# Kernel tuning notes

Hardware: AMD Instinct MI355X
Metric: run time of the kernel (lower is better)

The kernel has to match this reference:

```python
import jax, jax.numpy as jnp
import numpy as np

B, S, HID = 2, 2048, 768
H, D = 12, 64  # heads_num, per_head_size


def setup_inputs() -> dict:
    key0 = jax.random.key(0)
    ks = jax.random.split(key0, 12)
    inp = {
        "key": jax.random.normal(ks[0], (B, S, HID), jnp.float32),
        "value": jax.random.normal(ks[1], (B, S, HID), jnp.float32),
        "query": jax.random.normal(ks[2], (B, S, HID), jnp.float32),
        "mask": jnp.zeros((B, 1, S, S), jnp.float32),  # additive mask
        "position_bias": jax.random.normal(ks[3], (1, H, S, S), jnp.float32),
        "prev_attn": jax.random.normal(ks[4], (B, H, S, S), jnp.float32),
        "has_residual_attention": 1,
        # learned params (nn.Linear stores weight [out,in]; y = x @ W.T + b)
        "Wq": jax.random.normal(ks[5], (H * D, HID), jnp.float32) * 0.02,
        "bq": jnp.zeros((H * D,), jnp.float32),
        "Wk": jax.random.normal(ks[6], (H * D, HID), jnp.float32) * 0.02,
        "bk": jnp.zeros((H * D,), jnp.float32),
        "Wv": jax.random.normal(ks[7], (H * D, HID), jnp.float32) * 0.02,
        "bv": jnp.zeros((H * D,), jnp.float32),
        "Wo": jax.random.normal(ks[8], (HID, H * D), jnp.float32) * 0.02,
        "bo": jnp.zeros((HID,), jnp.float32),
    }
    return inp


def _heads(x, W, b):
    # [B,S,HID] -> [B,H,S,D]
    y = x @ W.T + b
    return y.reshape(B, S, H, D).transpose(0, 2, 1, 3)


def reference(key, value, query, mask, position_bias, prev_attn,
              has_residual_attention, Wq, bq, Wk, bk, Wv, bv, Wo, bo):
    q = _heads(query, Wq, bq)
    k = _heads(key, Wk, bk)
    v = _heads(value, Wv, bv)
    scores = jnp.einsum("bhqd,bhkd->bhqk", q, k)
    scores = scores + position_bias
    scores = scores / jnp.sqrt(jnp.float32(D))
    scores = scores + mask
    prev_attn_out = None
    if has_residual_attention:
        if prev_attn is not None:
            scores = scores + prev_attn
        prev_attn_out = scores
    probs = jax.nn.softmax(scores, axis=-1)  # dropout p=0.0 -> identity
    ctx = jnp.einsum("bhqk,bhkd->bhqd", probs, v)
    ctx = ctx.transpose(0, 2, 1, 3).reshape(B, S, H * D)
    out = ctx @ Wo.T + bo
    return (out, prev_attn_out)
```

## Files before the change

kernel.cpp:

```cpp
#include <hip/hip_runtime.h>
#include <hip/hip_bf16.h>

#define H_ 12
#define D_ 64
#define S_ 2048
#define B_ 2
#define HID_ 768

typedef short bf8 __attribute__((ext_vector_type(8)));
typedef float f4 __attribute__((ext_vector_type(4)));

#define MFMA(a,b,c) __builtin_amdgcn_mfma_f32_16x16x32_bf16(a,b,c,0,0,0)

__device__ __forceinline__ unsigned short f2bf(float f){
  __hip_bfloat16 h = __float2bfloat16(f);
  return __builtin_bit_cast(unsigned short, h);
}

__device__ __forceinline__ void st4bf(unsigned short* dst, float4 v){
  unsigned int u0 = (unsigned int)f2bf(v.x) | ((unsigned int)f2bf(v.y) << 16);
  unsigned int u1 = (unsigned int)f2bf(v.z) | ((unsigned int)f2bf(v.w) << 16);
  uint2 u; u.x = u0; u.y = u1;
  *reinterpret_cast<uint2*>(dst) = u;
}

__global__ __launch_bounds__(256) void proj_kernel(
    const float* __restrict__ Xq, const float* __restrict__ Xk, const float* __restrict__ Xv,
    const float* __restrict__ Wq_, const float* __restrict__ Wk_, const float* __restrict__ Wv_,
    const float* __restrict__ bq_, const float* __restrict__ bk_, const float* __restrict__ bv_,
    unsigned short* __restrict__ qb, unsigned short* __restrict__ kb,
    unsigned short* __restrict__ vtb)
{
  const int sel = blockIdx.z;
  const float* X    = sel==0 ? Xq  : (sel==1 ? Xk  : Xv);
  const float* W    = sel==0 ? Wq_ : (sel==1 ? Wk_ : Wv_);
  const float* bias = sel==0 ? bq_ : (sel==1 ? bk_ : bv_);
  const int m0 = blockIdx.x*64, n0 = blockIdx.y*64;
  __shared__ unsigned short lA[64*72];
  __shared__ unsigned short lB[64*72];
  const int tid = threadIdx.x;
  const int lane = tid & 63, w = tid >> 6;
  const int quad = lane >> 4, l16 = lane & 15;
  const int wm = (w>>1)*32, wn = (w&1)*32;
  f4 acc[2][2] = {};
  for (int k0=0; k0<HID_; k0+=64){
    #pragma unroll
    for (int i=0;i<4;i++){
      int idx = tid + i*256;
      int r = idx>>4, c4 = idx&15;
      float4 va = *reinterpret_cast<const float4*>(&X[(size_t)(m0+r)*HID_ + k0 + c4*4]);
      st4bf(&lA[r*72 + c4*4], va);
      float4 vb = *reinterpret_cast<const float4*>(&W[(size_t)(n0+r)*HID_ + k0 + c4*4]);
      st4bf(&lB[r*72 + c4*4], vb);
    }
    __syncthreads();
    #pragma unroll
    for (int kc=0;kc<2;kc++){
      bf8 a0 = *reinterpret_cast<const bf8*>(&lA[(wm    + l16)*72 + kc*32 + quad*8]);
      bf8 a1 = *reinterpret_cast<const bf8*>(&lA[(wm+16 + l16)*72 + kc*32 + quad*8]);
      bf8 b0 = *reinterpret_cast<const bf8*>(&lB[(wn    + l16)*72 + kc*32 + quad*8]);
      bf8 b1 = *reinterpret_cast<const bf8*>(&lB[(wn+16 + l16)*72 + kc*32 + quad*8]);
      acc[0][0] = MFMA(a0,b0,acc[0][0]);
      acc[0][1] = MFMA(a0,b1,acc[0][1]);
      acc[1][0] = MFMA(a1,b0,acc[1][0]);
      acc[1][1] = MFMA(a1,b1,acc[1][1]);
    }
    __syncthreads();
  }
  #pragma unroll
  for (int i=0;i<2;i++)
    #pragma unroll
    for (int j=0;j<2;j++)
      #pragma unroll
      for (int reg=0;reg<4;reg++){
        int row = m0 + wm + i*16 + quad*4 + reg;
        int col = n0 + wn + j*16 + l16;
        float val = acc[i][j][reg] + bias[col];
        int bb = row >> 11, s = row & 2047;
        int hh = col >> 6,  d = col & 63;
        unsigned short bv16 = f2bf(val);
        if (sel==0)      qb [((size_t)(bb*H_+hh)*S_ + s)*D_ + d] = bv16;
        else if (sel==1) kb [((size_t)(bb*H_+hh)*S_ + s)*D_ + d] = bv16;
        else             vtb[((size_t)(bb*H_+hh)*D_ + d)*S_ + s] = bv16;
      }
}

__global__ __launch_bounds__(256) void attn_kernel(
  const unsigned short* __restrict__ qb, const unsigned short* __restrict__ kb,
  const unsigned short* __restrict__ vtb,
  const float* __restrict__ pb, const float* __restrict__ msk,
  const float* __restrict__ prev, const int* __restrict__ flagp,
  float* __restrict__ prev_out, unsigned short* __restrict__ ctxb)
{
  const int qt = blockIdx.x, hh = blockIdx.y, bb = blockIdx.z;
  const int tid = threadIdx.x, w = tid>>6, lane = tid&63;
  const int quad = lane>>4, l16 = lane&15;
  const int flag = *flagp;
  __shared__ unsigned short lP[4*16*136];
  const int pbase = w*16*136;
  const unsigned short* Kb = kb  + (size_t)(bb*H_+hh)*S_*D_;
  const unsigned short* Vb = vtb + (size_t)(bb*H_+hh)*D_*S_;
  const unsigned short* Qb = qb  + (size_t)(bb*H_+hh)*S_*D_;
  const int q0 = qt*64;
  const int qq = q0 + w*16 + l16;
  bf8 qf0 = *reinterpret_cast<const bf8*>(&Qb[(size_t)qq*D_ + quad*8]);
  bf8 qf1 = *reinterpret_cast<const bf8*>(&Qb[(size_t)qq*D_ + 32 + quad*8]);
  const float* pbB = pb   + (size_t)hh*S_*S_;
  const float* mkB = msk  + (size_t)bb*S_*S_;
  const float* pvB = prev + (size_t)(bb*H_+hh)*S_*S_;
  float*       poB = prev_out + (size_t)(bb*H_+hh)*S_*S_;

  float m_run = -1e30f, l_run = 0.f;
  f4 O[4] = {};

  for (int kt=0; kt<S_; kt+=128){
    f4 sc[8];
    float mt = -1e30f;
    #pragma unroll
    for (int half=0; half<2; half++){
      f4 pbv[4], mkv[4], pvv[4];
      #pragma unroll
      for (int cc=0; cc<4; cc++){
        int c = half*4+cc;
        size_t off = (size_t)qq*S_ + kt + c*16 + quad*4;
        pbv[cc] = *reinterpret_cast<const f4*>(&pbB[off]);
        mkv[cc] = *reinterpret_cast<const f4*>(&mkB[off]);
      }
      if (flag){
        #pragma unroll
        for (int cc=0; cc<4; cc++){
          int c = half*4+cc;
          size_t off = (size_t)qq*S_ + kt + c*16 + quad*4;
          pvv[cc] = *reinterpret_cast<const f4*>(&pvB[off]);
        }
      } else {
        #pragma unroll
        for (int cc=0; cc<4; cc++){ pvv[cc][0]=0.f; pvv[cc][1]=0.f; pvv[cc][2]=0.f; pvv[cc][3]=0.f; }
      }
      #pragma unroll
      for (int cc=0; cc<4; cc++){
        int c = half*4+cc;
        const unsigned short* kr = &Kb[(size_t)(kt + c*16 + l16)*D_ + quad*8];
        bf8 k0v = *reinterpret_cast<const bf8*>(kr);
        bf8 k1v = *reinterpret_cast<const bf8*>(kr + 32);
        f4 z = {};
        z = MFMA(k0v, qf0, z);
        z = MFMA(k1v, qf1, z);
        sc[c] = z;
      }
      #pragma unroll
      for (int cc=0; cc<4; cc++){
        int c = half*4+cc;
        size_t off = (size_t)qq*S_ + kt + c*16 + quad*4;
        f4 vout;
        #pragma unroll
        for (int reg=0; reg<4; reg++){
          float v = (sc[c][reg] + pbv[cc][reg])*0.125f + mkv[cc][reg] + pvv[cc][reg];
          vout[reg] = v;
          mt = fmaxf(mt, v);
        }
        *reinterpret_cast<f4*>(&poB[off]) = vout;
        sc[c] = vout;
      }
    }
    mt = fmaxf(mt, __shfl_xor(mt, 16, 64));
    mt = fmaxf(mt, __shfl_xor(mt, 32, 64));
    float mn = fmaxf(m_run, mt);
    float al = __expf(m_run - mn);
    m_run = mn;
    float ps = 0.f;
    #pragma unroll
    for (int c=0;c<8;c++)
      #pragma unroll
      for (int reg=0;reg<4;reg++){
        float p = __expf(sc[c][reg] - mn);
        sc[c][reg] = p;
        ps += p;
      }
    ps += __shfl_xor(ps, 16, 64);
    ps += __shfl_xor(ps, 32, 64);
    l_run = l_run*al + ps;
    #pragma unroll
    for (int n=0;n<4;n++)
      #pragma unroll
      for (int reg=0;reg<4;reg++) O[n][reg] *= al;
    #pragma unroll
    for (int c=0;c<8;c++){
      unsigned int u0 = (unsigned int)f2bf(sc[c][0]) | ((unsigned int)f2bf(sc[c][1])<<16);
      unsigned int u1 = (unsigned int)f2bf(sc[c][2]) | ((unsigned int)f2bf(sc[c][3])<<16);
      uint2 u; u.x=u0; u.y=u1;
      *reinterpret_cast<uint2*>(&lP[pbase + l16*136 + c*16 + quad*4]) = u;
    }
    #pragma unroll
    for (int kb_=0;kb_<4;kb_++){
      bf8 pa = *reinterpret_cast<const bf8*>(&lP[pbase + l16*136 + kb_*32 + quad*8]);
      #pragma unroll
      for (int n=0;n<4;n++){
        bf8 vv = *reinterpret_cast<const bf8*>(&Vb[(size_t)(n*16+l16)*S_ + kt + kb_*32 + quad*8]);
        O[n] = MFMA(vv, pa, O[n]);
      }
    }
  }
  float rcp = 1.f / l_run;
  #pragma unroll
  for (int n=0;n<4;n++){
    unsigned int u0 = (unsigned int)f2bf(O[n][0]*rcp) | ((unsigned int)f2bf(O[n][1]*rcp)<<16);
    unsigned int u1 = (unsigned int)f2bf(O[n][2]*rcp) | ((unsigned int)f2bf(O[n][3]*rcp)<<16);
    uint2 u; u.x=u0; u.y=u1;
    *reinterpret_cast<uint2*>(&ctxb[(size_t)(bb*S_+qq)*HID_ + hh*D_ + n*16 + quad*4]) = u;
  }
}

__global__ __launch_bounds__(256) void outproj_kernel(
  const unsigned short* __restrict__ ctxb, const float* __restrict__ Wo,
  const float* __restrict__ bo, float* __restrict__ out)
{
  const int m0 = blockIdx.x*64, n0 = blockIdx.y*64;
  __shared__ unsigned short lA[64*72];
  __shared__ unsigned short lB[64*72];
  const int tid = threadIdx.x;
  const int lane = tid&63, w = tid>>6;
  const int quad = lane>>4, l16 = lane&15;
  const int wm = (w>>1)*32, wn = (w&1)*32;
  f4 acc[2][2] = {};
  for (int k0=0;k0<HID_;k0+=64){
    #pragma unroll
    for (int i=0;i<2;i++){
      int idx = tid + i*256;
      int r = idx>>3, c8 = idx&7;
      *reinterpret_cast<uint4*>(&lA[r*72 + c8*8]) =
        *reinterpret_cast<const uint4*>(&ctxb[(size_t)(m0+r)*HID_ + k0 + c8*8]);
    }
    #pragma unroll
    for (int i=0;i<4;i++){
      int idx = tid + i*256;
      int r = idx>>4, c4 = idx&15;
      float4 vb = *reinterpret_cast<const float4*>(&Wo[(size_t)(n0+r)*HID_ + k0 + c4*4]);
      st4bf(&lB[r*72 + c4*4], vb);
    }
    __syncthreads();
    #pragma unroll
    for (int kc=0;kc<2;kc++){
      bf8 a0 = *reinterpret_cast<const bf8*>(&lA[(wm    + l16)*72 + kc*32 + quad*8]);
      bf8 a1 = *reinterpret_cast<const bf8*>(&lA[(wm+16 + l16)*72 + kc*32 + quad*8]);
      bf8 b0 = *reinterpret_cast<const bf8*>(&lB[(wn    + l16)*72 + kc*32 + quad*8]);
      bf8 b1 = *reinterpret_cast<const bf8*>(&lB[(wn+16 + l16)*72 + kc*32 + quad*8]);
      acc[0][0] = MFMA(a0,b0,acc[0][0]);
      acc[0][1] = MFMA(a0,b1,acc[0][1]);
      acc[1][0] = MFMA(a1,b0,acc[1][0]);
      acc[1][1] = MFMA(a1,b1,acc[1][1]);
    }
    __syncthreads();
  }
  #pragma unroll
  for (int i=0;i<2;i++)
    #pragma unroll
    for (int j=0;j<2;j++)
      #pragma unroll
      for (int reg=0;reg<4;reg++){
        int row = m0 + wm + i*16 + quad*4 + reg;
        int col = n0 + wn + j*16 + l16;
        out[(size_t)row*HID_ + col] = acc[i][j][reg] + bo[col];
      }
}

extern "C" void kernel_launch(void* const* d_in, const int* in_sizes, int n_in,
                              void* d_out, int out_size, void* d_ws, size_t ws_size,
                              hipStream_t stream) {
  const float* key   = (const float*)d_in[0];
  const float* value = (const float*)d_in[1];
  const float* query = (const float*)d_in[2];
  const float* mask  = (const float*)d_in[3];
  const float* pbias = (const float*)d_in[4];
  const float* prev  = (const float*)d_in[5];
  const int*   flag  = (const int*)d_in[6];
  const float* Wq = (const float*)d_in[7];
  const float* bq = (const float*)d_in[8];
  const float* Wk = (const float*)d_in[9];
  const float* bk = (const float*)d_in[10];
  const float* Wv = (const float*)d_in[11];
  const float* bv = (const float*)d_in[12];
  const float* Wo = (const float*)d_in[13];
  const float* bo = (const float*)d_in[14];

  const size_t NQKV = (size_t)B_*H_*S_*D_;
  unsigned short* qbuf  = (unsigned short*)d_ws;
  unsigned short* kbuf  = qbuf  + NQKV;
  unsigned short* vtbuf = kbuf  + NQKV;
  unsigned short* ctxb  = vtbuf + NQKV;

  float* out = (float*)d_out;
  float* prev_out = out + (size_t)B_*S_*HID_;

  proj_kernel<<<dim3(64,12,3), 256, 0, stream>>>(
      query, key, value, Wq, Wk, Wv, bq, bk, bv, qbuf, kbuf, vtbuf);
  attn_kernel<<<dim3(S_/64, H_, B_), 256, 0, stream>>>(
      qbuf, kbuf, vtbuf, pbias, mask, prev, flag, prev_out, ctxb);
  outproj_kernel<<<dim3(64,12), 256, 0, stream>>>(ctxb, Wo, bo, out);
}
```

Measured before the change: 1.156 ms.

## Remap attention blocks across XCDs and hoist K/V/bias loads ahead of compute

Blocks are remapped so that consecutive hardware block IDs, which land on different XCDs, are spread so each XCD gets a contiguous range of (batch, head, q-tile) work, keeping K/V reuse within one L2. Inside the key loop, all K fragments, position-bias and mask loads for the 128-key tile are issued up front, and the V fragments are loaded into registers before the softmax. This gives more memory-level parallelism and hides global load latency behind the MFMA and exp work. The cost is much higher register pressure, which may cut occupancy or cause spills.

```diff
diff --git a/kernel.cpp b/kernel.cpp
--- a/kernel.cpp
+++ b/kernel.cpp
@@ -92,7 +92,12 @@
   const float* __restrict__ prev, const int* __restrict__ flagp,
   float* __restrict__ prev_out, unsigned short* __restrict__ ctxb)
 {
-  const int qt = blockIdx.x, hh = blockIdx.y, bb = blockIdx.z;
+  const int lin = blockIdx.x + 32*blockIdx.y + 384*blockIdx.z;
+  const int wg  = (lin & 7)*96 + (lin >> 3);
+  const int qt  = wg & 31;
+  const int hb  = wg >> 5;
+  const int bb  = (hb >= H_) ? 1 : 0;
+  const int hh  = hb - bb*H_;
   const int tid = threadIdx.x, w = tid>>6, lane = tid&63;
   const int quad = lane>>4, l16 = lane&15;
   const int flag = *flagp;
@@ -114,55 +119,65 @@
   f4 O[4] = {};
 
   for (int kt=0; kt<S_; kt+=128){
+    bf8 kv0[8], kv1[8];
+    #pragma unroll
+    for (int c=0;c<8;c++){
+      const unsigned short* kr = &Kb[(size_t)(kt + c*16 + l16)*D_ + quad*8];
+      kv0[c] = *reinterpret_cast<const bf8*>(kr);
+      kv1[c] = *reinterpret_cast<const bf8*>(kr + 32);
+    }
+    f4 pbv[8], mkv[8];
+    #pragma unroll
+    for (int c=0;c<8;c++){
+      size_t off = (size_t)qq*S_ + kt + c*16 + quad*4;
+      pbv[c] = *reinterpret_cast<const f4*>(&pbB[off]);
+      mkv[c] = *reinterpret_cast<const f4*>(&mkB[off]);
+    }
     f4 sc[8];
+    #pragma unroll
+    for (int c=0;c<8;c++){
+      f4 z = {};
+      z = MFMA(kv0[c], qf0, z);
+      z = MFMA(kv1[c], qf1, z);
+      sc[c] = z;
+    }
+    f4 pvv[8];
+    if (flag){
+      #pragma unroll
+      for (int c=0;c<8;c++){
+        size_t off = (size_t)qq*S_ + kt + c*16 + quad*4;
+        pvv[c] = *reinterpret_cast<const f4*>(&pvB[off]);
+      }
+    } else {
+      #pragma unroll
+      for (int c=0;c<8;c++){ pvv[c][0]=0.f; pvv[c][1]=0.f; pvv[c][2]=0.f; pvv[c][3]=0.f; }
+    }
+    #pragma unroll
+    for (int c=0;c<8;c++)
+      #pragma unroll
+      for (int reg=0;reg<4;reg++)
+        sc[c][reg] = (sc[c][reg] + pbv[c][reg])*0.125f + mkv[c][reg];
     float mt = -1e30f;
     #pragma unroll
-    for (int half=0; half<2; half++){
-      f4 pbv[4], mkv[4], pvv[4];
-      #pragma unroll
-      for (int cc=0; cc<4; cc++){
-        int c = half*4+cc;
-        size_t off = (size_t)qq*S_ + kt + c*16 + quad*4;
-        pbv[cc] = *reinterpret_cast<const f4*>(&pbB[off]);
-        mkv[cc] = *reinterpret_cast<const f4*>(&mkB[off]);
-      }
-      if (flag){
-        #pragma unroll
-        for (int cc=0; cc<4; cc++){
-          int c = half*4+cc;
-          size_t off = (size_t)qq*S_ + kt + c*16 + quad*4;
-          pvv[cc] = *reinterpret_cast<const f4*>(&pvB[off]);
-        }
-      } else {
-        #pragma unroll
-        for (int cc=0; cc<4; cc++){ pvv[cc][0]=0.f; pvv[cc][1]=0.f; pvv[cc][2]=0.f; pvv[cc][3]=0.f; }
-      }
-      #pragma unroll
-      for (int cc=0; cc<4; cc++){
-        int c = half*4+cc;
-        const unsigned short* kr = &Kb[(size_t)(kt + c*16 + l16)*D_ + quad*8];
-        bf8 k0v = *reinterpret_cast<const bf8*>(kr);
-        bf8 k1v = *reinterpret_cast<const bf8*>(kr + 32);
-        f4 z = {};
-        z = MFMA(k0v, qf0, z);
-        z = MFMA(k1v, qf1, z);
-        sc[c] = z;
-      }
-      #pragma unroll
-      for (int cc=0; cc<4; cc++){
-        int c = half*4+cc;
-        size_t off = (size_t)qq*S_ + kt + c*16 + quad*4;
-        f4 vout;
-        #pragma unroll
-        for (int reg=0; reg<4; reg++){
-          float v = (sc[c][reg] + pbv[cc][reg])*0.125f + mkv[cc][reg] + pvv[cc][reg];
-          vout[reg] = v;
-          mt = fmaxf(mt, v);
-        }
-        *reinterpret_cast<f4*>(&poB[off]) = vout;
-        sc[c] = vout;
-      }
-    }
+    for (int c=0;c<8;c++){
+      size_t off = (size_t)qq*S_ + kt + c*16 + quad*4;
+      f4 vout;
+      #pragma unroll
+      for (int reg=0;reg<4;reg++){
+        float v = sc[c][reg] + pvv[c][reg];
+        vout[reg] = v;
+        mt = fmaxf(mt, v);
+      }
+      *reinterpret_cast<f4*>(&poB[off]) = vout;
+      sc[c] = vout;
+    }
+    bf8 vvr[4][4];
+    #pragma unroll
+    for (int kb_=0;kb_<4;kb_++)
+      #pragma unroll
+      for (int n=0;n<4;n++)
+        vvr[kb_][n] = *reinterpret_cast<const bf8*>(
+            &Vb[(size_t)(n*16+l16)*S_ + kt + kb_*32 + quad*8]);
     mt = fmaxf(mt, __shfl_xor(mt, 16, 64));
     mt = fmaxf(mt, __shfl_xor(mt, 32, 64));
     float mn = fmaxf(m_run, mt);
@@ -195,10 +210,8 @@
     for (int kb_=0;kb_<4;kb_++){
       bf8 pa = *reinterpret_cast<const bf8*>(&lP[pbase + l16*136 + kb_*32 + quad*8]);
       #pragma unroll
-      for (int n=0;n<4;n++){
-        bf8 vv = *reinterpret_cast<const bf8*>(&Vb[(size_t)(n*16+l16)*S_ + kt + kb_*32 + quad*8]);
-        O[n] = MFMA(vv, pa, O[n]);
-      }
+      for (int n=0;n<4;n++)
+        O[n] = MFMA(vvr[kb_][n], pa, O[n]);
     }
   }
   float rcp = 1.f / l_run;
```

New measurement: 1.130 ms. 1.02x faster.
